# Optimization experiments

Measured on AMD Instinct MI355X. Metric: run time of the kernel, lower is better.

The kernel has to match this reference:

```python
import jax, jax.numpy as jnp
import numpy as np

EMBED = 768
HEADS = 12
HEAD_DIM = EMBED // HEADS
RANK = 16
EPS = 1e-6
SCALE = 1.0 / np.sqrt(HEAD_DIM)


def setup_inputs() -> dict:
    key = jax.random.key(0)
    ks = jax.random.split(key, 12)
    B, S = 4, 1024
    hidden_states = jax.random.normal(ks[0], (B, S, EMBED), dtype=jnp.float32)
    attention_mask = jnp.zeros((B, 1, 1, S), dtype=jnp.float32)
    w = lambda k: jax.random.normal(k, (EMBED, EMBED), dtype=jnp.float32) * 0.02
    b = lambda k: jax.random.normal(k, (EMBED,), dtype=jnp.float32) * 0.02
    A = jax.random.normal(ks[9], (HEADS, HEAD_DIM, RANK), dtype=jnp.float32) * 0.05
    return {
        "hidden_states": hidden_states,
        "attention_mask": attention_mask,
        "Wq": w(ks[1]), "bq": b(ks[2]),
        "Wk": w(ks[3]), "bk": b(ks[4]),
        "Wv": w(ks[5]), "bv": b(ks[6]),
        "Wo": w(ks[7]), "bo": b(ks[8]),
        "A": A,
    }


def reference(hidden_states, attention_mask, Wq, bq, Wk, bk, Wv, bv, Wo, bo, A):
    B, S, E = hidden_states.shape
    H, D = HEADS, HEAD_DIM

    def proj(W, bias):
        y = hidden_states @ W.T + bias          # (B,S,E), torch Linear: x W^T + b
        return y.reshape(B, S, H, D).transpose(0, 2, 1, 3)  # (B,H,S,D)

    q = proj(Wq, bq)
    k = proj(Wk, bk)
    v = proj(Wv, bv)

    # Low-rank SPD Mahalanobis: G_h = A_h A_h^T + eps*I
    # d^2(x,y) = ||A^T(x-y)||^2 + eps*||x-y||^2 (block-diagonal per batch)
    qA = jnp.einsum("bhsd,hdr->bhsr", q, A)    # (B,H,S,R)
    kA = jnp.einsum("bhsd,hdr->bhsr", k, A)
    qq = jnp.sum(qA * qA, -1) + EPS * jnp.sum(q * q, -1)  # (B,H,S)
    kk = jnp.sum(kA * kA, -1) + EPS * jnp.sum(k * k, -1)
    cross = jnp.einsum("bhsr,bhtr->bhst", qA, kA) + EPS * jnp.einsum("bhsd,bhtd->bhst", q, k)
    d2 = qq[..., :, None] + kk[..., None, :] - 2.0 * cross  # (B,H,S,S)

    scores = -d2 * SCALE + attention_mask      # mask broadcasts (B,1,1,S)
    weights = jax.nn.softmax(scores, axis=-1)  # dropout p is identity in eval
    ctx = jnp.einsum("bhst,bhtd->bhsd", weights, v)
    ctx = ctx.transpose(0, 2, 1, 3).reshape(B, S, E)
    return ctx @ Wo.T + bo
```

## Files before the change

### kernel.cpp

```cpp
#include <hip/hip_runtime.h>

typedef __attribute__((ext_vector_type(8))) short s16x8;
typedef __attribute__((ext_vector_type(4))) float f32x4;
typedef __attribute__((ext_vector_type(4))) unsigned int u32x4;
typedef __attribute__((ext_vector_type(2))) unsigned int u32x2;
typedef unsigned short u16;
typedef unsigned int u32;
typedef unsigned long long u64;

__device__ __forceinline__ u16 f2bf(float f) {
  u32 u = __float_as_uint(f);
  u32 r = u + 0x7fffu + ((u >> 16) & 1u);
  return (u16)(r >> 16);
}
__device__ __forceinline__ float bf2f(u16 h) {
  return __uint_as_float(((u32)h) << 16);
}

typedef __attribute__((address_space(3))) char lds_char_t;
typedef __attribute__((address_space(1))) const char glb_char_t;
__device__ __forceinline__ void gl2lds16(const void* g, void* l) {
  __builtin_amdgcn_global_load_lds((glb_char_t*)g, (lds_char_t*)l, 16, 0, 0);
}

#define HS_N 3145728
#define W_N  589824
#define LOG2E 1.44269504f

__global__ __launch_bounds__(256) void convert_kernel(
    const float* __restrict__ hs, const float* __restrict__ wq, const float* __restrict__ wk,
    const float* __restrict__ wv, const float* __restrict__ wo,
    const float* __restrict__ bq, const float* __restrict__ bk, const float* __restrict__ bv,
    u16* __restrict__ hsb, u16* __restrict__ wqkvb, u16* __restrict__ wob,
    float* __restrict__ biasqkv)
{
  int t = blockIdx.x * 256 + threadIdx.x;
  long i = (long)t * 8;
  const float* src;
  u16* dst;
  if (i < HS_N)              { src = hs + i;                  dst = hsb + i; }
  else if (i < HS_N + W_N)   { src = wq + (i - HS_N);         dst = wqkvb + (i - HS_N); }
  else if (i < HS_N + 2*W_N) { src = wk + (i - HS_N - W_N);   dst = wqkvb + (i - HS_N); }
  else if (i < HS_N + 3*W_N) { src = wv + (i - HS_N - 2*W_N); dst = wqkvb + (i - HS_N); }
  else                       { src = wo + (i - HS_N - 3*W_N); dst = wob + (i - HS_N - 3*W_N); }
  float4 a = ((const float4*)src)[0];
  float4 b = ((const float4*)src)[1];
  uint4 o;
  o.x = (u32)f2bf(a.x) | ((u32)f2bf(a.y) << 16);
  o.y = (u32)f2bf(a.z) | ((u32)f2bf(a.w) << 16);
  o.z = (u32)f2bf(b.x) | ((u32)f2bf(b.y) << 16);
  o.w = (u32)f2bf(b.z) | ((u32)f2bf(b.w) << 16);
  *(uint4*)dst = o;
  if (t < 2304) biasqkv[t] = (t < 768) ? bq[t] : ((t < 1536) ? bk[t - 768] : bv[t - 1536]);
}

template<int MODE>
__global__ __launch_bounds__(256, 2) void gemm_bt(
    const u16* __restrict__ A, const u16* __restrict__ Bt, const float* __restrict__ bias,
    float* __restrict__ outF, u16* __restrict__ Qb, u16* __restrict__ Kb, u16* __restrict__ Vtb)
{
  constexpr int NT = (MODE == 0) ? 18 : 6;
  constexpr int CPX = NT * 64 / 8;

  __shared__ __align__(16) char sm[73728];
  char* const smA = sm;
  char* const smB = sm + 24576;

  const int tid = threadIdx.x;
  const int lane = tid & 63;
  const int w = tid >> 6;
  const int l15 = lane & 15, g = lane >> 4;
  const int wid = (blockIdx.x & 7) * CPX + (blockIdx.x >> 3);
  const int bx = wid % NT, by = wid / NT;
  const int mBase = by * 64;
  const int nBase = bx * 128;
  const int wr = w >> 1, wc = w & 1;
  const int mW = wr * 32, nW = wc * 64;

  f32x4 zero = {0.f, 0.f, 0.f, 0.f};
  f32x4 acc[2][4];
  #pragma unroll
  for (int i = 0; i < 2; i++)
    #pragma unroll
    for (int j = 0; j < 4; j++) acc[i][j] = zero;

  const u16* Arow = A + (long)mBase * 768;
  const u16* Brow = Bt + (long)nBase * 768;

  auto stage = [&](int c, int kb) {
    const int k0 = c * 64;
    #pragma unroll
    for (int i = 0; i < 2; i++) {
      int o = (i * 256 + tid) * 16;
      int r = o >> 7;
      int sl = ((o >> 4) & 7) ^ (r & 7);
      gl2lds16(Arow + (long)r * 768 + k0 + sl * 8,
               smA + kb * 8192 + i * 4096 + w * 1024);
    }
    #pragma unroll
    for (int i = 0; i < 4; i++) {
      int o = (i * 256 + tid) * 16;
      int r = o >> 7;
      int sl = ((o >> 4) & 7) ^ (r & 7);
      gl2lds16(Brow + (long)r * 768 + k0 + sl * 8,
               smB + kb * 16384 + i * 4096 + w * 1024);
    }
  };

  auto compute = [&](int kb) {
    const char* bufA = smA + kb * 8192;
    const char* bufB = smB + kb * 16384;
    #pragma unroll
    for (int kh = 0; kh < 2; kh++) {
      s16x8 af[2], bf[4];
      #pragma unroll
      for (int mi = 0; mi < 2; mi++) {
        int R = mW + mi * 16 + l15;
        af[mi] = *(const s16x8*)(bufA + R * 128 + (((kh * 4 + g) ^ (l15 & 7)) << 4));
      }
      #pragma unroll
      for (int ni = 0; ni < 4; ni++) {
        int R = nW + ni * 16 + l15;
        bf[ni] = *(const s16x8*)(bufB + R * 128 + (((kh * 4 + g) ^ (l15 & 7)) << 4));
      }
      #pragma unroll
      for (int mi = 0; mi < 2; mi++)
        #pragma unroll
        for (int ni = 0; ni < 4; ni++)
          acc[mi][ni] = __builtin_amdgcn_mfma_f32_16x16x32_bf16(af[mi], bf[ni], acc[mi][ni], 0, 0, 0);
    }
  };

  auto body = [&](int c, int kb, int kbn) {
    if (c < 11) { stage(c + 1, kbn); asm volatile("s_waitcnt vmcnt(6)" ::: "memory"); }
    else        { asm volatile("s_waitcnt vmcnt(0)" ::: "memory"); }
    asm volatile("s_barrier" ::: "memory");
    compute(kb);
  };

  stage(0, 0);
  #pragma unroll 1
  for (int cc = 0; cc < 4; cc++) {
    body(cc * 3,     0, 1);
    body(cc * 3 + 1, 1, 2);
    body(cc * 3 + 2, 2, 0);
  }
  __syncthreads();

  const int b_ = mBase >> 10;
  const int s0b = mBase & 1023;

  if constexpr (MODE == 1) {
    #pragma unroll
    for (int mi = 0; mi < 2; mi++)
      #pragma unroll
      for (int ni = 0; ni < 4; ni++) {
        int n = nBase + nW + ni * 16 + l15;
        int m0 = mBase + mW + mi * 16 + g * 4;
        float bb = bias[n];
        outF[(long)m0 * 768 + n]       = acc[mi][ni][0] + bb;
        outF[(long)(m0 + 1) * 768 + n] = acc[mi][ni][1] + bb;
        outF[(long)(m0 + 2) * 768 + n] = acc[mi][ni][2] + bb;
        outF[(long)(m0 + 3) * 768 + n] = acc[mi][ni][3] + bb;
      }
  } else {
    const int typ = bx / 6;
    if (typ < 2) {
      u16* qk = (typ == 0) ? Qb : Kb;
      #pragma unroll
      for (int mi = 0; mi < 2; mi++)
        #pragma unroll
        for (int ni = 0; ni < 4; ni++) {
          int n = nBase + nW + ni * 16 + l15;
          int hn = n - typ * 768;
          int h = hn >> 6, d = hn & 63;
          long bh = (long)b_ * 12 + h;
          int s0 = s0b + mW + mi * 16 + g * 4;
          float bb = bias[n];
          u16* dst = qk + (bh << 16) + ((long)s0 << 6) + d;
          dst[0]   = f2bf(acc[mi][ni][0] + bb);
          dst[64]  = f2bf(acc[mi][ni][1] + bb);
          dst[128] = f2bf(acc[mi][ni][2] + bb);
          dst[192] = f2bf(acc[mi][ni][3] + bb);
        }
    } else {
      u16* ct = (u16*)sm;
      #pragma unroll
      for (int mi = 0; mi < 2; mi++)
        #pragma unroll
        for (int ni = 0; ni < 4; ni++) {
          int nr = nW + ni * 16 + l15;
          int mr = mW + mi * 16 + g * 4;
          float bb = bias[nBase + nr];
          u32 lo = (u32)f2bf(acc[mi][ni][0] + bb) | ((u32)f2bf(acc[mi][ni][1] + bb) << 16);
          u32 hi = (u32)f2bf(acc[mi][ni][2] + bb) | ((u32)f2bf(acc[mi][ni][3] + bb) << 16);
          *(u64*)(ct + nr * 72 + mr) = (u64)lo | ((u64)hi << 32);
        }
      __syncthreads();
      int dr = tid >> 1, part = tid & 1;
      int hn = (bx - 12) * 128 + dr;
      int h = hn >> 6, d = hn & 63;
      long bh = (long)b_ * 12 + h;
      u16* dst = Vtb + (bh << 16) + (d << 10) + s0b + part * 32;
      const u16* srl = ct + dr * 72 + part * 32;
      #pragma unroll
      for (int i = 0; i < 4; i++)
        *(uint4*)(dst + i * 8) = *(const uint4*)(srl + i * 8);
    }
  }
}

__global__ __launch_bounds__(256) void qk_ext_kernel(
    const u16* __restrict__ Qb, const u16* __restrict__ Kb, const float* __restrict__ Am,
    const float* __restrict__ mask, u16* __restrict__ qAe, u16* __restrict__ kAe,
    float* __restrict__ beta2)
{
  const bool isK = blockIdx.x >= 192;
  const int rb = blockIdx.x * 256 - (isK ? 49152 : 0);
  const int h = (rb >> 10) % 12;
  const int row = rb + threadIdx.x;
  const int bh = row >> 10;
  const int s = row & 1023;
  const int b_ = bh / 12;

  const u16* src = (isK ? Kb : Qb) + ((long)row << 6);
  union { uint4 v4[8]; u32 u[32]; } c;
  #pragma unroll
  for (int i = 0; i < 8; i++) c.v4[i] = ((const uint4*)src)[i];

  const float* Ah = Am + h * 1024;
  float acc[16];
  #pragma unroll
  for (int r = 0; r < 16; r++) acc[r] = 0.f;
  float s2 = 0.f;
  #pragma unroll
  for (int d = 0; d < 64; d++) {
    u32 wd = c.u[d >> 1];
    float qd = bf2f((u16)((d & 1) ? (wd >> 16) : (wd & 0xffffu)));
    s2 += qd * qd;
    #pragma unroll
    for (int r = 0; r < 16; r++) acc[r] += qd * Ah[d * 16 + r];
  }

  union { u16 us[128]; uint4 v4[16]; } o;
  const float sA = isK ? 1.0f : 0.25f * LOG2E;
  const float sQ = isK ? 1e-3f : 0.25e-3f * LOG2E;
  #pragma unroll
  for (int r = 0; r < 16; r++) o.us[r] = f2bf(acc[r] * sA);
  #pragma unroll
  for (int d = 0; d < 64; d++) {
    u32 wd = c.u[d >> 1];
    float qd = bf2f((u16)((d & 1) ? (wd >> 16) : (wd & 0xffffu)));
    o.us[16 + d] = f2bf(qd * sQ);
  }
  #pragma unroll
  for (int j = 80; j < 128; j++) o.us[j] = 0;

  u16* dst = (isK ? kAe : qAe) + ((long)row << 7);
  #pragma unroll
  for (int i = 0; i < 16; i++) ((uint4*)dst)[i] = o.v4[i];

  if (isK) {
    float kk = 1e-6f * s2;
    #pragma unroll
    for (int r = 0; r < 16; r++) kk += acc[r] * acc[r];
    beta2[row] = LOG2E * (-0.125f * kk + mask[(b_ << 10) + s]);
  }
}

__global__ __launch_bounds__(128, 2) void attn_kernel(
    const u16* __restrict__ qAe, const u16* __restrict__ kAe, const u16* __restrict__ Vtb,
    const float* __restrict__ beta2, u16* __restrict__ ctxb)
{
  const int tid = threadIdx.x;
  const int lane = tid & 63;
  const int w = tid >> 6;
  const int l15 = lane & 15, g = lane >> 4;
  const int wid = ((int)blockIdx.x & 7) * 96 + ((int)blockIdx.x >> 3);
  const int bh = wid >> 4;
  const int qt = wid & 15;
  const int q0 = qt * 64 + w * 32;

  __shared__ __align__(16) char sm[46080];
  char* const kb0  = sm;
  char* const kb1  = sm + 16384;
  char* const Pw   = sm + 32768 + w * 4608;
  float* const Blds = (float*)(sm + 41984);

  const u16* qbase = qAe + ((long)(bh * 1024 + q0) << 7);
  const u16* kbase = kAe + ((long)bh << 17);
  const u16* vbase = Vtb + ((long)bh << 16);
  const float* betab = beta2 + (bh << 10);

  u32x4 bqv[2][3];
  #pragma unroll
  for (int qf = 0; qf < 2; qf++)
    #pragma unroll
    for (int ks = 0; ks < 3; ks++) {
      const u16* a = qbase + ((qf * 16 + l15) << 7) + ks * 32 + g * 8;
      asm volatile("global_load_dwordx4 %0, %1, off" : "=v"(bqv[qf][ks]) : "v"(a));
    }
  #pragma unroll
  for (int i = 0; i < 4; i++)
    gl2lds16(betab + i * 256 + lane * 4, (char*)Blds + i * 1024);

  auto stageK = [&](int c, char* buf) {
    const int t0 = c * 64;
    #pragma unroll
    for (int i2 = 0; i2 < 8; i2++) {
      int i = w * 8 + i2;
      int r = i * 4 + (lane >> 4);
      int col = ((lane & 15) ^ (r & 7)) * 8;
      gl2lds16(kbase + (long)(t0 + r) * 128 + col, buf + i * 1024);
    }
  };
  auto loadV = [&](int c, u32x4 (&dst)[8]) {
    const int t0 = c * 64;
    #pragma unroll
    for (int ks2 = 0; ks2 < 2; ks2++)
      #pragma unroll
      for (int df = 0; df < 4; df++) {
        const u16* a = vbase + ((df * 16 + l15) << 10) + t0 + ks2 * 32 + g * 8;
        asm volatile("global_load_dwordx4 %0, %1, off" : "=v"(dst[ks2 * 4 + df]) : "v"(a));
      }
  };

  f32x4 zero = {0.f, 0.f, 0.f, 0.f};
  f32x4 cacc[2][4];
  #pragma unroll
  for (int a = 0; a < 2; a++)
    #pragma unroll
    for (int b = 0; b < 4; b++) cacc[a][b] = zero;
  float rsum[2] = {0.f, 0.f};
  u32x4 vb[8];

  stageK(0, kb0);

  std::integral_constant<bool, false> Ff;
  std::integral_constant<bool, true>  Tt;

  auto iter = [&](auto LASTC, int c, const char* bufc, char* bufn) {
    constexpr bool LAST = decltype(LASTC)::value;
    loadV(c, vb);
    asm volatile("s_waitcnt vmcnt(8)" ::: "memory");
    asm volatile("s_barrier" ::: "memory");
    __builtin_amdgcn_sched_barrier(0);
    if constexpr (!LAST) stageK(c + 1, bufn);
    f32x4 sacc[4][2];
    #pragma unroll
    for (int tf = 0; tf < 4; tf++) { sacc[tf][0] = zero; sacc[tf][1] = zero; }
    #pragma unroll
    for (int tf = 0; tf < 4; tf++)
      #pragma unroll
      for (int ks = 0; ks < 3; ks++) {
        s16x8 ak = *(const s16x8*)(bufc + (tf * 16 + l15) * 256 +
                                   ((ks * 64 + g * 16) ^ ((l15 & 7) << 4)));
        s16x8 b0 = __builtin_bit_cast(s16x8, bqv[0][ks]);
        s16x8 b1 = __builtin_bit_cast(s16x8, bqv[1][ks]);
        sacc[tf][0] = __builtin_amdgcn_mfma_f32_16x16x32_bf16(ak, b0, sacc[tf][0], 0, 0, 0);
        sacc[tf][1] = __builtin_amdgcn_mfma_f32_16x16x32_bf16(ak, b1, sacc[tf][1], 0, 0, 0);
      }
    if constexpr (!LAST) asm volatile("s_waitcnt vmcnt(8)" ::: "memory");
    else                 asm volatile("s_waitcnt vmcnt(0)" ::: "memory");
    __builtin_amdgcn_sched_barrier(0);
    #pragma unroll
    for (int tf = 0; tf < 4; tf++) {
      f32x4 bb = *(const f32x4*)((const char*)Blds + c * 256 + tf * 64 + g * 16);
      #pragma unroll
      for (int qf = 0; qf < 2; qf++) {
        float e0, e1, e2, e3;
        asm("v_exp_f32 %0, %1" : "=v"(e0) : "v"(sacc[tf][qf][0] + bb[0]));
        asm("v_exp_f32 %0, %1" : "=v"(e1) : "v"(sacc[tf][qf][1] + bb[1]));
        asm("v_exp_f32 %0, %1" : "=v"(e2) : "v"(sacc[tf][qf][2] + bb[2]));
        asm("v_exp_f32 %0, %1" : "=v"(e3) : "v"(sacc[tf][qf][3] + bb[3]));
        rsum[qf] += (e0 + e1) + (e2 + e3);
        u32 p01, p23;
        asm("v_cvt_pk_bf16_f32 %0, %1, %2" : "=v"(p01) : "v"(e0), "v"(e1));
        asm("v_cvt_pk_bf16_f32 %0, %1, %2" : "=v"(p23) : "v"(e2), "v"(e3));
        u32x2 pk = {p01, p23};
        *(u32x2*)(Pw + (qf * 16 + l15) * 144 + tf * 32 + g * 8) = pk;
      }
    }
    #pragma unroll
    for (int qf = 0; qf < 2; qf++)
      #pragma unroll
      for (int ks2 = 0; ks2 < 2; ks2++) {
        s16x8 ap = *(const s16x8*)(Pw + (qf * 16 + l15) * 144 + ks2 * 64 + g * 16);
        #pragma unroll
        for (int df = 0; df < 4; df++) {
          s16x8 bv = __builtin_bit_cast(s16x8, vb[ks2 * 4 + df]);
          cacc[qf][df] = __builtin_amdgcn_mfma_f32_16x16x32_bf16(ap, bv, cacc[qf][df], 0, 0, 0);
        }
      }
  };

  #pragma unroll 1
  for (int c2 = 0; c2 < 7; c2++) {
    iter(Ff, 2 * c2,     kb0, kb1);
    iter(Ff, 2 * c2 + 1, kb1, kb0);
  }
  iter(Ff, 14, kb0, kb1);
  iter(Tt, 15, kb1, kb0);

  #pragma unroll
  for (int qf = 0; qf < 2; qf++) {
    rsum[qf] += __shfl_xor(rsum[qf], 16);
    rsum[qf] += __shfl_xor(rsum[qf], 32);
  }
  const int b_ = bh / 12, h = bh % 12;
  #pragma unroll
  for (int qf = 0; qf < 2; qf++) {
    #pragma unroll
    for (int j = 0; j < 4; j++) {
      float rs = __shfl(rsum[qf], g * 4 + j);
      float rinv = 1.0f / rs;
      int qg = q0 + qf * 16 + g * 4 + j;
      long base = ((long)(b_ * 1024 + qg)) * 768 + h * 64;
      #pragma unroll
      for (int df = 0; df < 4; df++)
        ctxb[base + df * 16 + l15] = f2bf(cacc[qf][df][j] * rinv);
    }
  }
}

extern "C" void kernel_launch(void* const* d_in, const int* in_sizes, int n_in,
                              void* d_out, int out_size, void* d_ws, size_t ws_size,
                              hipStream_t stream)
{
  (void)in_sizes; (void)n_in; (void)out_size; (void)ws_size;
  const float* hs   = (const float*)d_in[0];
  const float* mask = (const float*)d_in[1];
  const float* Wq   = (const float*)d_in[2];
  const float* bq   = (const float*)d_in[3];
  const float* Wk   = (const float*)d_in[4];
  const float* bk   = (const float*)d_in[5];
  const float* Wv   = (const float*)d_in[6];
  const float* bv   = (const float*)d_in[7];
  const float* Wo   = (const float*)d_in[8];
  const float* bo   = (const float*)d_in[9];
  const float* Am   = (const float*)d_in[10];
  float* out = (float*)d_out;

  char* p = (char*)d_ws;
  u16* hsb      = (u16*)p;   p += 6291456;
  u16* wqkvb    = (u16*)p;   p += 3538944;
  u16* wob      = (u16*)p;   p += 1179648;
  float* biasqkv= (float*)p; p += 9216;
  u16* Qb       = (u16*)p;   p += 6291456;
  u16* Kb       = (u16*)p;   p += 6291456;
  u16* Vtb      = (u16*)p;   p += 6291456;
  u16* qAeb     = (u16*)p;   p += 12582912;
  u16* kAeb     = (u16*)p;   p += 12582912;
  float* beta2  = (float*)p; p += 196608;
  u16* ctxb     = (u16*)p;   p += 6291456;

  convert_kernel<<<2688, 256, 0, stream>>>(hs, Wq, Wk, Wv, Wo, bq, bk, bv,
                                           hsb, wqkvb, wob, biasqkv);
  gemm_bt<0><<<1152, 256, 0, stream>>>(hsb, wqkvb, biasqkv,
                                       nullptr, Qb, Kb, Vtb);
  qk_ext_kernel<<<384, 256, 0, stream>>>(Qb, Kb, Am, mask, qAeb, kAeb, beta2);
  attn_kernel<<<768, 128, 0, stream>>>(qAeb, kAeb, Vtb, beta2, ctxb);
  gemm_bt<1><<<384, 256, 0, stream>>>(ctxb, wob, bo, out,
                                      nullptr, nullptr, nullptr);
}
```

Baseline: 95.25 us.

## Fuse low-rank Q/K extension into QKV projection GEMM epilogue

Removes the separate qk_ext_kernel and the intermediate Q/K bf16 buffers. The QKV GEMM epilogue for Q and K tiles now stages results in shared memory, computes the A-projection, scaled copies and beta2 with two threads per row, and writes the extended qAe/kAe layout directly. This drops one launch and a 12 MB write plus read round trip. In exchange the GEMM epilogue gets heavier (per-thread 16x32 FMA loops and global reads of A), which could add register pressure and latency to the GEMM.

```diff
diff --git a/kernel.cpp b/kernel.cpp
--- a/kernel.cpp
+++ b/kernel.cpp
@@ -57,7 +57,9 @@
 template<int MODE>
 __global__ __launch_bounds__(256, 2) void gemm_bt(
     const u16* __restrict__ A, const u16* __restrict__ Bt, const float* __restrict__ bias,
-    float* __restrict__ outF, u16* __restrict__ Qb, u16* __restrict__ Kb, u16* __restrict__ Vtb)
+    float* __restrict__ outF, u16* __restrict__ Vtb, const float* __restrict__ Am,
+    const float* __restrict__ maskp, u16* __restrict__ qAe, u16* __restrict__ kAe,
+    float* __restrict__ beta2)
 {
   constexpr int NT = (MODE == 0) ? 18 : 6;
   constexpr int CPX = NT * 64 / 8;
@@ -165,25 +167,7 @@
       }
   } else {
     const int typ = bx / 6;
-    if (typ < 2) {
-      u16* qk = (typ == 0) ? Qb : Kb;
-      #pragma unroll
-      for (int mi = 0; mi < 2; mi++)
-        #pragma unroll
-        for (int ni = 0; ni < 4; ni++) {
-          int n = nBase + nW + ni * 16 + l15;
-          int hn = n - typ * 768;
-          int h = hn >> 6, d = hn & 63;
-          long bh = (long)b_ * 12 + h;
-          int s0 = s0b + mW + mi * 16 + g * 4;
-          float bb = bias[n];
-          u16* dst = qk + (bh << 16) + ((long)s0 << 6) + d;
-          dst[0]   = f2bf(acc[mi][ni][0] + bb);
-          dst[64]  = f2bf(acc[mi][ni][1] + bb);
-          dst[128] = f2bf(acc[mi][ni][2] + bb);
-          dst[192] = f2bf(acc[mi][ni][3] + bb);
-        }
-    } else {
+    if (typ == 2) {
       u16* ct = (u16*)sm;
       #pragma unroll
       for (int mi = 0; mi < 2; mi++)
@@ -206,65 +190,71 @@
       #pragma unroll
       for (int i = 0; i < 4; i++)
         *(uint4*)(dst + i * 8) = *(const uint4*)(srl + i * 8);
-    }
-  }
-}
-
-__global__ __launch_bounds__(256) void qk_ext_kernel(
-    const u16* __restrict__ Qb, const u16* __restrict__ Kb, const float* __restrict__ Am,
-    const float* __restrict__ mask, u16* __restrict__ qAe, u16* __restrict__ kAe,
-    float* __restrict__ beta2)
-{
-  const bool isK = blockIdx.x >= 192;
-  const int rb = blockIdx.x * 256 - (isK ? 49152 : 0);
-  const int h = (rb >> 10) % 12;
-  const int row = rb + threadIdx.x;
-  const int bh = row >> 10;
-  const int s = row & 1023;
-  const int b_ = bh / 12;
-
-  const u16* src = (isK ? Kb : Qb) + ((long)row << 6);
-  union { uint4 v4[8]; u32 u[32]; } c;
-  #pragma unroll
-  for (int i = 0; i < 8; i++) c.v4[i] = ((const uint4*)src)[i];
-
-  const float* Ah = Am + h * 1024;
-  float acc[16];
-  #pragma unroll
-  for (int r = 0; r < 16; r++) acc[r] = 0.f;
-  float s2 = 0.f;
-  #pragma unroll
-  for (int d = 0; d < 64; d++) {
-    u32 wd = c.u[d >> 1];
-    float qd = bf2f((u16)((d & 1) ? (wd >> 16) : (wd & 0xffffu)));
-    s2 += qd * qd;
-    #pragma unroll
-    for (int r = 0; r < 16; r++) acc[r] += qd * Ah[d * 16 + r];
-  }
-
-  union { u16 us[128]; uint4 v4[16]; } o;
-  const float sA = isK ? 1.0f : 0.25f * LOG2E;
-  const float sQ = isK ? 1e-3f : 0.25e-3f * LOG2E;
-  #pragma unroll
-  for (int r = 0; r < 16; r++) o.us[r] = f2bf(acc[r] * sA);
-  #pragma unroll
-  for (int d = 0; d < 64; d++) {
-    u32 wd = c.u[d >> 1];
-    float qd = bf2f((u16)((d & 1) ? (wd >> 16) : (wd & 0xffffu)));
-    o.us[16 + d] = f2bf(qd * sQ);
-  }
-  #pragma unroll
-  for (int j = 80; j < 128; j++) o.us[j] = 0;
-
-  u16* dst = (isK ? kAe : qAe) + ((long)row << 7);
-  #pragma unroll
-  for (int i = 0; i < 16; i++) ((uint4*)dst)[i] = o.v4[i];
-
-  if (isK) {
-    float kk = 1e-6f * s2;
-    #pragma unroll
-    for (int r = 0; r < 16; r++) kk += acc[r] * acc[r];
-    beta2[row] = LOG2E * (-0.125f * kk + mask[(b_ << 10) + s]);
+    } else {
+      u16* cl = (u16*)sm;
+      #pragma unroll
+      for (int mi = 0; mi < 2; mi++)
+        #pragma unroll
+        for (int ni = 0; ni < 4; ni++) {
+          int nr = nW + ni * 16 + l15;
+          int mr = mW + mi * 16 + g * 4;
+          float bb = bias[nBase + nr];
+          cl[(mr + 0) * 130 + nr] = f2bf(acc[mi][ni][0] + bb);
+          cl[(mr + 1) * 130 + nr] = f2bf(acc[mi][ni][1] + bb);
+          cl[(mr + 2) * 130 + nr] = f2bf(acc[mi][ni][2] + bb);
+          cl[(mr + 3) * 130 + nr] = f2bf(acc[mi][ni][3] + bb);
+        }
+      __syncthreads();
+      const bool isK = (typ == 1);
+      const int rowid = tid >> 1, dh = tid & 1;
+      const int sl = rowid & 63, hh = rowid >> 6;
+      const u16* crow = cl + sl * 130 + hh * 64 + dh * 32;
+      const int h = (bx - typ * 6) * 2 + hh;
+      const float* Ah = Am + h * 1024 + dh * 512;
+      float qa[16];
+      #pragma unroll
+      for (int r = 0; r < 16; r++) qa[r] = 0.f;
+      float s2 = 0.f;
+      #pragma unroll
+      for (int dd = 0; dd < 32; dd++) {
+        float qd = bf2f(crow[dd]);
+        s2 += qd * qd;
+        #pragma unroll
+        for (int r = 0; r < 16; r++) qa[r] += qd * Ah[dd * 16 + r];
+      }
+      #pragma unroll
+      for (int r = 0; r < 16; r++) qa[r] += __shfl_xor(qa[r], 1);
+      s2 += __shfl_xor(s2, 1);
+      const float sA_ = isK ? 1.0f : 0.25f * LOG2E;
+      const float sQ_ = isK ? 1e-3f : 0.25e-3f * LOG2E;
+      const int s0 = s0b + sl;
+      const long bhq = (long)b_ * 12 + h;
+      u16* dst = (isK ? kAe : qAe) + (((bhq << 10) + s0) << 7);
+      uint4 z = {0, 0, 0, 0};
+      if (dh == 0) {
+        union { u16 us[48]; uint4 v4[6]; } ob;
+        #pragma unroll
+        for (int r = 0; r < 16; r++) ob.us[r] = f2bf(qa[r] * sA_);
+        #pragma unroll
+        for (int dd = 0; dd < 32; dd++) ob.us[16 + dd] = f2bf(bf2f(crow[dd]) * sQ_);
+        #pragma unroll
+        for (int i = 0; i < 6; i++) ((uint4*)dst)[i] = ob.v4[i];
+        ((uint4*)dst)[10] = z; ((uint4*)dst)[11] = z; ((uint4*)dst)[12] = z;
+        if (isK) {
+          float kk = 1e-6f * s2;
+          #pragma unroll
+          for (int r = 0; r < 16; r++) kk += qa[r] * qa[r];
+          beta2[(bhq << 10) + s0] = LOG2E * (-0.125f * kk + maskp[(b_ << 10) + s0]);
+        }
+      } else {
+        union { u16 us[32]; uint4 v4[4]; } ob;
+        #pragma unroll
+        for (int dd = 0; dd < 32; dd++) ob.us[dd] = f2bf(bf2f(crow[dd]) * sQ_);
+        #pragma unroll
+        for (int i = 0; i < 4; i++) ((uint4*)dst)[6 + i] = ob.v4[i];
+        ((uint4*)dst)[13] = z; ((uint4*)dst)[14] = z; ((uint4*)dst)[15] = z;
+      }
+    }
   }
 }
 
@@ -446,8 +436,6 @@
   u16* wqkvb    = (u16*)p;   p += 3538944;
   u16* wob      = (u16*)p;   p += 1179648;
   float* biasqkv= (float*)p; p += 9216;
-  u16* Qb       = (u16*)p;   p += 6291456;
-  u16* Kb       = (u16*)p;   p += 6291456;
   u16* Vtb      = (u16*)p;   p += 6291456;
   u16* qAeb     = (u16*)p;   p += 12582912;
   u16* kAeb     = (u16*)p;   p += 12582912;
@@ -456,10 +444,9 @@
 
   convert_kernel<<<2688, 256, 0, stream>>>(hs, Wq, Wk, Wv, Wo, bq, bk, bv,
                                            hsb, wqkvb, wob, biasqkv);
-  gemm_bt<0><<<1152, 256, 0, stream>>>(hsb, wqkvb, biasqkv,
-                                       nullptr, Qb, Kb, Vtb);
-  qk_ext_kernel<<<384, 256, 0, stream>>>(Qb, Kb, Am, mask, qAeb, kAeb, beta2);
+  gemm_bt<0><<<1152, 256, 0, stream>>>(hsb, wqkvb, biasqkv, nullptr,
+                                       Vtb, Am, mask, qAeb, kAeb, beta2);
   attn_kernel<<<768, 128, 0, stream>>>(qAeb, kAeb, Vtb, beta2, ctxb);
   gemm_bt<1><<<384, 256, 0, stream>>>(ctxb, wob, bo, out,
-                                      nullptr, nullptr, nullptr);
-}
+                                      nullptr, nullptr, nullptr, nullptr, nullptr, nullptr);
+}
```

Result: slower. 109.4 us (+14.8%).

## Double-buffer V register prefetch in attention and stage A matrix in LDS

Applied to the files above, without the earlier changes.

The attention kernel now prefetches the next chunk's V tile into a second register set one iteration ahead, so V loads overlap a full iteration of QK and softmax work rather than being waited on mid-iteration. The occupancy hint changes from launch_bounds min-blocks to waves_per_eu(1,2), giving the compiler room for the extra VGPRs. The qk_ext kernel copies the per-head A matrix into LDS and reads it with vector loads instead of scalar global loads. The doubled V registers raise register pressure and may cut occupancy. The vmcnt(8) waits rely on the exact count of stageK loads in flight, which is not shown.

```diff
diff --git a/kernel.cpp b/kernel.cpp
--- a/kernel.cpp
+++ b/kernel.cpp
@@ -215,6 +215,7 @@
     const float* __restrict__ mask, u16* __restrict__ qAe, u16* __restrict__ kAe,
     float* __restrict__ beta2)
 {
+  __shared__ __align__(16) float AhL[1024];
   const bool isK = blockIdx.x >= 192;
   const int rb = blockIdx.x * 256 - (isK ? 49152 : 0);
   const int h = (rb >> 10) % 12;
@@ -223,12 +224,15 @@
   const int s = row & 1023;
   const int b_ = bh / 12;
 
+  ((float4*)AhL)[threadIdx.x] = ((const float4*)(Am + h * 1024))[threadIdx.x];
+
   const u16* src = (isK ? Kb : Qb) + ((long)row << 6);
   union { uint4 v4[8]; u32 u[32]; } c;
   #pragma unroll
   for (int i = 0; i < 8; i++) c.v4[i] = ((const uint4*)src)[i];
 
-  const float* Ah = Am + h * 1024;
+  __syncthreads();
+
   float acc[16];
   #pragma unroll
   for (int r = 0; r < 16; r++) acc[r] = 0.f;
@@ -239,7 +243,13 @@
     float qd = bf2f((u16)((d & 1) ? (wd >> 16) : (wd & 0xffffu)));
     s2 += qd * qd;
     #pragma unroll
-    for (int r = 0; r < 16; r++) acc[r] += qd * Ah[d * 16 + r];
+    for (int r4 = 0; r4 < 4; r4++) {
+      f32x4 a4 = *(const f32x4*)&AhL[d * 16 + r4 * 4];
+      acc[r4 * 4 + 0] += qd * a4[0];
+      acc[r4 * 4 + 1] += qd * a4[1];
+      acc[r4 * 4 + 2] += qd * a4[2];
+      acc[r4 * 4 + 3] += qd * a4[3];
+    }
   }
 
   union { u16 us[128]; uint4 v4[16]; } o;
@@ -268,7 +278,8 @@
   }
 }
 
-__global__ __launch_bounds__(128, 2) void attn_kernel(
+__global__ __attribute__((amdgpu_waves_per_eu(1, 2))) __launch_bounds__(128)
+void attn_kernel(
     const u16* __restrict__ qAe, const u16* __restrict__ kAe, const u16* __restrict__ Vtb,
     const float* __restrict__ beta2, u16* __restrict__ ctxb)
 {
@@ -332,17 +343,24 @@
     #pragma unroll
     for (int b = 0; b < 4; b++) cacc[a][b] = zero;
   float rsum[2] = {0.f, 0.f};
-  u32x4 vb[8];
+  u32x4 vA[8], vB[8];
 
   stageK(0, kb0);
+  __builtin_amdgcn_sched_barrier(0);
+  loadV(0, vA);
 
   std::integral_constant<bool, false> Ff;
   std::integral_constant<bool, true>  Tt;
 
-  auto iter = [&](auto LASTC, int c, const char* bufc, char* bufn) {
+  auto iter = [&](auto LASTC, int c, const char* bufc, char* bufn,
+                  u32x4 (&vcur)[8], u32x4 (&vnxt)[8]) {
     constexpr bool LAST = decltype(LASTC)::value;
-    loadV(c, vb);
-    asm volatile("s_waitcnt vmcnt(8)" ::: "memory");
+    if constexpr (!LAST) {
+      loadV(c + 1, vnxt);
+      asm volatile("s_waitcnt vmcnt(8)" ::: "memory");
+    } else {
+      asm volatile("s_waitcnt vmcnt(0)" ::: "memory");
+    }
     asm volatile("s_barrier" ::: "memory");
     __builtin_amdgcn_sched_barrier(0);
     if constexpr (!LAST) stageK(c + 1, bufn);
@@ -360,9 +378,6 @@
         sacc[tf][0] = __builtin_amdgcn_mfma_f32_16x16x32_bf16(ak, b0, sacc[tf][0], 0, 0, 0);
         sacc[tf][1] = __builtin_amdgcn_mfma_f32_16x16x32_bf16(ak, b1, sacc[tf][1], 0, 0, 0);
       }
-    if constexpr (!LAST) asm volatile("s_waitcnt vmcnt(8)" ::: "memory");
-    else                 asm volatile("s_waitcnt vmcnt(0)" ::: "memory");
-    __builtin_amdgcn_sched_barrier(0);
     #pragma unroll
     for (int tf = 0; tf < 4; tf++) {
       f32x4 bb = *(const f32x4*)((const char*)Blds + c * 256 + tf * 64 + g * 16);
@@ -388,7 +403,7 @@
         s16x8 ap = *(const s16x8*)(Pw + (qf * 16 + l15) * 144 + ks2 * 64 + g * 16);
         #pragma unroll
         for (int df = 0; df < 4; df++) {
-          s16x8 bv = __builtin_bit_cast(s16x8, vb[ks2 * 4 + df]);
+          s16x8 bv = __builtin_bit_cast(s16x8, vcur[ks2 * 4 + df]);
           cacc[qf][df] = __builtin_amdgcn_mfma_f32_16x16x32_bf16(ap, bv, cacc[qf][df], 0, 0, 0);
         }
       }
@@ -396,11 +411,11 @@
 
   #pragma unroll 1
   for (int c2 = 0; c2 < 7; c2++) {
-    iter(Ff, 2 * c2,     kb0, kb1);
-    iter(Ff, 2 * c2 + 1, kb1, kb0);
-  }
-  iter(Ff, 14, kb0, kb1);
-  iter(Tt, 15, kb1, kb0);
+    iter(Ff, 2 * c2,     kb0, kb1, vA, vB);
+    iter(Ff, 2 * c2 + 1, kb1, kb0, vB, vA);
+  }
+  iter(Ff, 14, kb0, kb1, vA, vB);
+  iter(Tt, 15, kb1, kb0, vB, vA);
 
   #pragma unroll
   for (int qf = 0; qf < 2; qf++) {
```

Result: slower. 107.6 us (+12.9%).
